# Kernel tuning notes

Hardware: AMD Instinct MI355X
Metric: run time of the kernel (lower is better)

The kernel has to match this reference:

```python
import jax, jax.numpy as jnp
import numpy as np

B, N, D = 8, 4096, 256
H = W = 64          # grid_size = img_size // patch_size = 256 // 4
WS = 8              # swin window size
NH = 8              # swin heads
M = 16              # fno modes
E = 4               # num experts
TD = 768            # text dim
HID = 1024          # mlp hidden = 4 * D
TK = 2              # top_k


def gelu(x):
    return jax.nn.gelu(x, approximate=False)


def layernorm(x, g, b, eps=1e-5):
    mu = x.mean(-1, keepdims=True)
    var = ((x - mu) ** 2).mean(-1, keepdims=True)
    return (x - mu) * jax.lax.rsqrt(var + eps) * g + b


def fno_expert(x, w1r, w1i, w2r, w2i, conv_w, conv_b):
    # x: [B, N, D] -> grid [B, D, H, W]
    xg = x.transpose(0, 2, 1).reshape(B, D, H, W)
    xft = jnp.fft.rfft2(xg)                      # [B, D, H, W//2+1] complex64
    w1 = w1r + 1j * w1i
    w2 = w2r + 1j * w2i
    top = jnp.einsum('bixy,ioxy->boxy', xft[:, :, :M, :M], w1)
    bot = jnp.einsum('bixy,ioxy->boxy', xft[:, :, -M:, :M], w2)
    out_ft = jnp.zeros((B, D, H, W // 2 + 1), dtype=xft.dtype)
    out_ft = out_ft.at[:, :, :M, :M].set(top).at[:, :, -M:, :M].set(bot)
    x1 = jnp.fft.irfft2(out_ft, s=(H, W))        # [B, D, H, W]
    x2 = jnp.einsum('bdhw,do->bohw', xg, conv_w) + conv_b[None, :, None, None]
    out = gelu(x1 + x2)
    return out.reshape(B, D, N).transpose(0, 2, 1) + x


def mlp_expert(x, w1, b1, w2, b2):
    return gelu(x @ w1 + b1) @ w2 + b2 + x


def window_attn_expert(x, ln1_g, ln1_b, qkv_w, qkv_b, out_w, out_b,
                       ln2_g, ln2_b, mw1, mb1, mw2, mb2):
    shortcut = x
    h = layernorm(x, ln1_g, ln1_b)
    # window partition: [B,H,W,C] -> [B*nW, WS*WS, C]
    h = h.reshape(B, H // WS, WS, W // WS, WS, D)
    h = h.transpose(0, 1, 3, 2, 4, 5).reshape(-1, WS * WS, D)
    # multi-head self attention (torch nn.MultiheadAttention semantics)
    qkv = h @ qkv_w + qkv_b                      # [Bw, L, 3D]
    q, k, v = jnp.split(qkv, 3, axis=-1)
    dh = D // NH
    def heads(t):
        return t.reshape(-1, WS * WS, NH, dh).transpose(0, 2, 1, 3)
    q, k, v = heads(q), heads(k), heads(v)
    scores = jnp.einsum('whld,whmd->whlm', q, k) / jnp.sqrt(jnp.float32(dh))
    attn = jax.nn.softmax(scores, axis=-1)
    o = jnp.einsum('whlm,whmd->whld', attn, v)
    o = o.transpose(0, 2, 1, 3).reshape(-1, WS * WS, D)
    o = o @ out_w + out_b
    # window reverse
    o = o.reshape(B, H // WS, W // WS, WS, WS, D)
    o = o.transpose(0, 1, 3, 2, 4, 5).reshape(B, N, D)
    x = o + shortcut
    h2 = layernorm(x, ln2_g, ln2_b)
    return x + (gelu(h2 @ mw1 + mb1) @ mw2 + mb2)


def setup_inputs() -> dict:
    key = jax.random.key(0)
    ks = jax.random.split(key, 24)
    rn = lambda k, s: jax.random.normal(k, s, jnp.float32) * 0.02
    fscale = 1.0 / (D * D)
    ru = lambda k: jax.random.uniform(k, (D, D, M, M), jnp.float32) * fscale
    return {
        'x': jax.random.normal(ks[0], (B, N, D), jnp.float32),
        'text_embedding': jax.random.normal(ks[1], (B, TD), jnp.float32),
        'gate_w1': rn(ks[2], (D + TD, D)), 'gate_b1': jnp.zeros((D,), jnp.float32),
        'gate_w2': rn(ks[3], (D, E)), 'gate_b2': jnp.zeros((E,), jnp.float32),
        'fno_w1r': ru(ks[4]), 'fno_w1i': ru(ks[5]),
        'fno_w2r': ru(ks[6]), 'fno_w2i': ru(ks[7]),
        'fno_conv_w': rn(ks[8], (D, D)), 'fno_conv_b': jnp.zeros((D,), jnp.float32),
        'mlp1_w1': rn(ks[9], (D, HID)), 'mlp1_b1': jnp.zeros((HID,), jnp.float32),
        'mlp1_w2': rn(ks[10], (HID, D)), 'mlp1_b2': jnp.zeros((D,), jnp.float32),
        'mlp2_w1': rn(ks[11], (D, HID)), 'mlp2_b1': jnp.zeros((HID,), jnp.float32),
        'mlp2_w2': rn(ks[12], (HID, D)), 'mlp2_b2': jnp.zeros((D,), jnp.float32),
        'wa_ln1_g': jnp.ones((D,), jnp.float32), 'wa_ln1_b': jnp.zeros((D,), jnp.float32),
        'wa_qkv_w': rn(ks[13], (D, 3 * D)), 'wa_qkv_b': jnp.zeros((3 * D,), jnp.float32),
        'wa_out_w': rn(ks[14], (D, D)), 'wa_out_b': jnp.zeros((D,), jnp.float32),
        'wa_ln2_g': jnp.ones((D,), jnp.float32), 'wa_ln2_b': jnp.zeros((D,), jnp.float32),
        'wa_mlp_w1': rn(ks[15], (D, HID)), 'wa_mlp_b1': jnp.zeros((HID,), jnp.float32),
        'wa_mlp_w2': rn(ks[16], (HID, D)), 'wa_mlp_b2': jnp.zeros((D,), jnp.float32),
    }


def reference(x, text_embedding, gate_w1, gate_b1, gate_w2, gate_b2,
              fno_w1r, fno_w1i, fno_w2r, fno_w2i, fno_conv_w, fno_conv_b,
              mlp1_w1, mlp1_b1, mlp1_w2, mlp1_b2,
              mlp2_w1, mlp2_b1, mlp2_w2, mlp2_b2,
              wa_ln1_g, wa_ln1_b, wa_qkv_w, wa_qkv_b, wa_out_w, wa_out_b,
              wa_ln2_g, wa_ln2_b, wa_mlp_w1, wa_mlp_b1, wa_mlp_w2, wa_mlp_b2):
    # --- gating ---
    feat = jnp.concatenate([x.mean(axis=1), text_embedding], axis=1)  # [B, D+TD]
    logits = jax.nn.relu(feat @ gate_w1 + gate_b1) @ gate_w2 + gate_b2  # [B, E]
    top_v, top_i = jax.lax.top_k(logits, TK)
    weights = jax.nn.softmax(top_v, axis=-1)                           # [B, TK]
    # per-expert combined weight: cw[b,e] = sum_k w[b,k] * (idx[b,k]==e)
    cw = (jax.nn.one_hot(top_i, E, dtype=x.dtype) * weights[..., None]).sum(axis=1)  # [B, E]
    # --- experts (FNO, MLP, WindowAttn, MLP) ---
    e0 = fno_expert(x, fno_w1r, fno_w1i, fno_w2r, fno_w2i, fno_conv_w, fno_conv_b)
    e1 = mlp_expert(x, mlp1_w1, mlp1_b1, mlp1_w2, mlp1_b2)
    e2 = window_attn_expert(x, wa_ln1_g, wa_ln1_b, wa_qkv_w, wa_qkv_b,
                            wa_out_w, wa_out_b, wa_ln2_g, wa_ln2_b,
                            wa_mlp_w1, wa_mlp_b1, wa_mlp_w2, wa_mlp_b2)
    e3 = mlp_expert(x, mlp2_w1, mlp2_b1, mlp2_w2, mlp2_b2)
    outs = jnp.stack([e0, e1, e2, e3])                                 # [E, B, N, D]
    final = jnp.einsum('be,ebnd->bnd', cw, outs)
    return final, weights
```

## Files before the change

### kernel.cpp

```cpp
#include <hip/hip_runtime.h>
#include <math.h>


#define NB 8
#define NN 4096
#define DD 256

typedef __attribute__((ext_vector_type(8))) short bf16x8;
typedef __attribute__((ext_vector_type(4))) float f32x4;

__device__ __forceinline__ float gelu_f(float v) {
    return 0.5f * v * (1.0f + erff(v * 0.7071067811865475f));
}
__device__ __forceinline__ ushort f2bf(float f) {
    uint32_t u = __float_as_uint(f);
    uint32_t r = (u + 0x7fffu + ((u >> 16) & 1u)) >> 16;
    return (ushort)r;
}
__device__ __forceinline__ float b2f(ushort h) {
    return __uint_as_float(((uint32_t)h) << 16);
}

__global__ void k_gate_mean1(const float* __restrict__ x, float* __restrict__ partial) {
    int c = blockIdx.x, b = blockIdx.y;
    int t = threadIdx.x;
    const float* xb = x + ((size_t)b * NN + c * 128) * DD;
    float s = 0.f;
    for (int n = 0; n < 128; ++n) s += xb[(size_t)n * DD + t];
    partial[((size_t)b * 32 + c) * 256 + t] = s;
}
__global__ void k_gate_mean2(const float* __restrict__ partial, const float* __restrict__ text,
                             float* __restrict__ feat) {
    int b = blockIdx.x, t = threadIdx.x;
    float s = 0.f;
    for (int c = 0; c < 32; ++c) s += partial[((size_t)b * 32 + c) * 256 + t];
    feat[b * 1024 + t] = s * (1.0f / NN);
    for (int j = t; j < 768; j += 256) feat[b * 1024 + 256 + j] = text[b * 768 + j];
}

__global__ void k_gate_mlp1(const float* __restrict__ feat, const float* __restrict__ w1,
                            const float* __restrict__ b1, float* __restrict__ h1) {
    int b = blockIdx.x, j = threadIdx.x;
    float acc = b1[j];
    const float* f = feat + b * 1024;
    for (int k = 0; k < 1024; ++k) acc += f[k] * w1[k * 256 + j];
    h1[b * 256 + j] = fmaxf(acc, 0.f);
}

__global__ void k_gate_top(const float* __restrict__ h1, const float* __restrict__ w2,
                           const float* __restrict__ b2, float* __restrict__ cw,
                           float* __restrict__ wout) {
    __shared__ float lg[8][4];
    int t = threadIdx.x;
    if (t < 32) {
        int b = t >> 2, e = t & 3;
        float acc = b2[e];
        const float* h = h1 + b * 256;
        for (int k = 0; k < 256; ++k) acc += h[k] * w2[k * 4 + e];
        lg[b][e] = acc;
    }
    __syncthreads();
    if (t < 8) {
        int b = t;
        float v[4];
        #pragma unroll
        for (int e = 0; e < 4; ++e) v[e] = lg[b][e];
        int i0 = 0;
        #pragma unroll
        for (int e = 1; e < 4; ++e) if (v[e] > v[i0]) i0 = e;
        int i1 = -1;
        #pragma unroll
        for (int e = 0; e < 4; ++e) {
            if (e == i0) continue;
            if (i1 < 0 || v[e] > v[i1]) i1 = e;
        }
        float v0 = v[i0], v1 = v[i1];
        float e1v = expf(v1 - v0);
        float inv = 1.0f / (1.0f + e1v);
        float w0 = inv, w1v = e1v * inv;
        wout[b * 2 + 0] = w0;
        wout[b * 2 + 1] = w1v;
        float c[4] = {0.f, 0.f, 0.f, 0.f};
        c[i0] += w0; c[i1] += w1v;
        #pragma unroll
        for (int e = 0; e < 4; ++e) cw[b * 4 + e] = c[e];
    }
}

__global__ void k_cvtbf(const float* __restrict__ src, ushort* __restrict__ dst) {
    int i = blockIdx.x * 256 + threadIdx.x;
    float4 v = ((const float4*)src)[i];
    ushort4 o;
    o.x = f2bf(v.x); o.y = f2bf(v.y); o.z = f2bf(v.z); o.w = f2bf(v.w);
    ((ushort4*)dst)[i] = o;
}

__global__ void k_wt(const float* __restrict__ src, ushort* __restrict__ dst, int K, int N) {
    __shared__ float tile[32][33];
    int n0 = blockIdx.x * 32, k0 = blockIdx.y * 32;
    int tx = threadIdx.x, ty = threadIdx.y;
    #pragma unroll
    for (int i = 0; i < 4; ++i)
        tile[ty + i * 8][tx] = src[(size_t)(k0 + ty + i * 8) * N + n0 + tx];
    __syncthreads();
    #pragma unroll
    for (int i = 0; i < 4; ++i)
        dst[(size_t)(n0 + ty + i * 8) * K + k0 + tx] = f2bf(tile[tx][ty + i * 8]);
}

template<int MODE>
__global__ void __launch_bounds__(256) k_gemm(const ushort* __restrict__ A,
        const ushort* __restrict__ Bt, const float* __restrict__ bias,
        const float* __restrict__ res, float* __restrict__ outf,
        ushort* __restrict__ outb, const float* __restrict__ cw, int eidx,
        int K, int Ncols, size_t bsA, size_t bsB, size_t bsC) {
    __shared__ alignas(16) char smem[32768];
    ushort* sA = (ushort*)smem;
    ushort* sB = (ushort*)(smem + 16384);
    int z = blockIdx.z;
    A += z * bsA; Bt += z * bsB;
    if (outf) outf += z * bsC;
    if (outb) outb += z * bsC;
    int m0 = blockIdx.x * 128;
    int n0 = blockIdx.y * 128;
    int t = threadIdx.x;
    int lane = t & 63, wid = t >> 6;
    int wr = wid >> 1, wc = wid & 1;
    int rlo = lane & 15, khi = (lane >> 4) * 8;

    auto stage = [&](int buf, int k0) {
        const ushort* Ab = A + (size_t)m0 * K + k0;
        const ushort* Bb = Bt + (size_t)n0 * K + k0;
        #pragma unroll
        for (int h = 0; h < 2; ++h) {
            int s = t + h * 256;
            int row = s >> 2, kc = (s & 3) * 8;
            __builtin_amdgcn_global_load_lds(
                (const __attribute__((address_space(1))) void*)(Ab + (size_t)row * K + kc),
                (__attribute__((address_space(3))) void*)(sA + buf * 4096 + s * 8),
                16, 0, 0);
            __builtin_amdgcn_global_load_lds(
                (const __attribute__((address_space(1))) void*)(Bb + (size_t)row * K + kc),
                (__attribute__((address_space(3))) void*)(sB + buf * 4096 + s * 8),
                16, 0, 0);
        }
    };

    f32x4 acc[4][4];
    #pragma unroll
    for (int i = 0; i < 4; ++i)
        #pragma unroll
        for (int j = 0; j < 4; ++j) acc[i][j] = (f32x4){0.f, 0.f, 0.f, 0.f};

    int KT = K >> 5;
    stage(0, 0);
    int cur = 0;
    for (int kt = 0; kt < KT; ++kt) {
        __syncthreads();
        if (kt + 1 < KT) stage(cur ^ 1, (kt + 1) << 5);
        const ushort* Ap = sA + cur * 4096;
        const ushort* Bp = sB + cur * 4096;
        bf16x8 af[4], bfr[4];
        #pragma unroll
        for (int i = 0; i < 4; ++i) {
            af[i]  = *(const bf16x8*)(Ap + (wr * 64 + i * 16 + rlo) * 32 + khi);
            bfr[i] = *(const bf16x8*)(Bp + (wc * 64 + i * 16 + rlo) * 32 + khi);
        }
        #pragma unroll
        for (int i = 0; i < 4; ++i)
            #pragma unroll
            for (int j = 0; j < 4; ++j)
                acc[i][j] = __builtin_amdgcn_mfma_f32_16x16x32_bf16(af[i], bfr[j], acc[i][j], 0, 0, 0);
        cur ^= 1;
    }

    float bj4[4];
    if constexpr (MODE != 4 && MODE != 5) {
        #pragma unroll
        for (int nt = 0; nt < 4; ++nt) bj4[nt] = bias[n0 + wc * 64 + nt * 16 + rlo];
    }

    if constexpr (MODE == 0 || MODE == 1 || MODE == 5) {
        ushort* eb = (ushort*)smem;
        #pragma unroll
        for (int mt = 0; mt < 4; ++mt) {
            __syncthreads();
            #pragma unroll
            for (int nt = 0; nt < 4; ++nt) {
                int col = wc * 64 + nt * 16 + rlo;
                #pragma unroll
                for (int j = 0; j < 4; ++j) {
                    float v = acc[mt][nt][j];
                    if constexpr (MODE == 5)
                        v += bias[m0 + wr * 64 + mt * 16 + (lane >> 4) * 4 + j];
                    else
                        v += bj4[nt];
                    if (MODE == 0) v = gelu_f(v);
                    eb[(wr * 16 + (lane >> 4) * 4 + j) * 136 + col] = f2bf(v);
                }
            }
            __syncthreads();
            #pragma unroll
            for (int h = 0; h < 2; ++h) {
                int s = t + h * 256;
                int r = s >> 4, c = (s & 15) * 8;
                int grow = m0 + (r >> 4) * 64 + mt * 16 + (r & 15);
                *(uint4*)(outb + (size_t)grow * Ncols + n0 + c) = *(uint4*)&eb[r * 136 + c];
            }
        }
    } else {
        float* ep = (float*)smem;
        #pragma unroll
        for (int mt = 0; mt < 4; ++mt) {
            __syncthreads();
            #pragma unroll
            for (int nt = 0; nt < 4; ++nt) {
                int col = wc * 64 + nt * 16 + rlo;
                #pragma unroll
                for (int j = 0; j < 4; ++j) {
                    float v = acc[mt][nt][j];
                    if constexpr (MODE == 4)
                        v += bias[m0 + wr * 64 + mt * 16 + (lane >> 4) * 4 + j];
                    else
                        v += bj4[nt];
                    ep[(wr * 16 + (lane >> 4) * 4 + j) * 132 + col] = v;
                }
            }
            __syncthreads();
            #pragma unroll
            for (int h = 0; h < 4; ++h) {
                int s = t + h * 256;
                int r = s >> 5, c4 = (s & 31) * 4;
                int grow = m0 + (r >> 4) * 64 + mt * 16 + (r & 15);
                size_t g = (size_t)grow * Ncols + n0 + c4;
                float4 v = *(float4*)&ep[r * 132 + c4];
                if constexpr (MODE == 2) {
                    if (res) {
                        float4 rv = *(const float4*)&res[g];
                        v.x += rv.x; v.y += rv.y; v.z += rv.z; v.w += rv.w;
                    }
                    *(float4*)&outf[g] = v;
                } else if constexpr (MODE == 4) {
                    *(float4*)&outf[g] = v;
                } else {
                    float cwv = cw[(grow >> 12) * 4 + eidx];
                    float4 rv = *(const float4*)&res[g];
                    float4 ov = *(float4*)&outf[g];
                    ov.x += cwv * (v.x + rv.x);
                    ov.y += cwv * (v.y + rv.y);
                    ov.z += cwv * (v.z + rv.z);
                    ov.w += cwv * (v.w + rv.w);
                    *(float4*)&outf[g] = ov;
                }
            }
        }
    }
}

__global__ void k_transpose(const float* __restrict__ x, float* __restrict__ xg) {
    __shared__ float tile[32][33];
    int b = blockIdx.z;
    int nt = blockIdx.x, dt = blockIdx.y;
    int tx = threadIdx.x, ty = threadIdx.y;
    const float* xb = x + (size_t)b * NN * DD;
    float* xgb = xg + (size_t)b * DD * NN;
    #pragma unroll
    for (int i = 0; i < 4; ++i) {
        int n = nt * 32 + ty + i * 8;
        tile[ty + i * 8][tx] = xb[(size_t)n * DD + dt * 32 + tx];
    }
    __syncthreads();
    #pragma unroll
    for (int i = 0; i < 4; ++i) {
        int d = dt * 32 + ty + i * 8;
        xgb[(size_t)d * NN + nt * 32 + tx] = tile[tx][ty + i * 8];
    }
}

__global__ void __launch_bounds__(64) k_rfft2(const float* __restrict__ xg, float* __restrict__ xft) {
    __shared__ float plane[64][65];
    __shared__ float s1[64][16][2];
    __shared__ float twc[64], tws[64];
    int p = blockIdx.x;
    int t = threadIdx.x;
    const float* src = xg + (size_t)p * 4096;
    for (int i = 0; i < 64; ++i) plane[i][t] = src[i * 64 + t];
    twc[t] = cosf((float)t * (6.283185307179586f / 64.0f));
    tws[t] = sinf((float)t * (6.283185307179586f / 64.0f));
    __syncthreads();
    int r = t;
    for (int kw = 0; kw < 16; ++kw) {
        float re = 0.f, im = 0.f;
        for (int w = 0; w < 64; ++w) {
            int j = (w * kw) & 63;
            float xv = plane[r][w];
            re += xv * twc[j];
            im -= xv * tws[j];
        }
        s1[r][kw][0] = re; s1[r][kw][1] = im;
    }
    __syncthreads();
    float2* dst = (float2*)xft + (size_t)p * 512;
    #pragma unroll
    for (int q = 0; q < 8; ++q) {
        int oi = t + q * 64;
        int krow = oi >> 4, kw = oi & 15;
        int kh = krow < 16 ? krow : krow + 32;
        float re = 0.f, im = 0.f;
        for (int h = 0; h < 64; ++h) {
            int j = (h * kh) & 63;
            float c = twc[j], s = tws[j];
            float ar = s1[h][kw][0], ai = s1[h][kw][1];
            re += ar * c + ai * s;
            im += ai * c - ar * s;
        }
        dst[oi] = make_float2(re, im);
    }
}

__global__ void __launch_bounds__(512) k_spectral(const float* __restrict__ xft,
        const float* __restrict__ w1r, const float* __restrict__ w1i,
        const float* __restrict__ w2r, const float* __restrict__ w2i,
        float* __restrict__ part) {
    __shared__ alignas(16) ushort Wl[32 * 648];
    __shared__ alignas(16) ushort Xl[16 * 648];
    int z = blockIdx.z;
    int region = z >> 1, is = z & 1;
    const float* wrp = region ? w2r : w1r;
    const float* wip = region ? w2i : w1i;
    int xm = blockIdx.y;
    int krow = region * 16 + xm;
    int o0 = blockIdx.x * 16;
    int t = threadIdx.x;
    int wv = t >> 6, lane = t & 63;
    int rlo = lane & 15, khi = lane >> 4;
    int ibase = is * 128;

    f32x4 acc[2][2];
    #pragma unroll
    for (int a = 0; a < 2; ++a)
        #pragma unroll
        for (int b = 0; b < 2; ++b) acc[a][b] = (f32x4){0.f, 0.f, 0.f, 0.f};

    for (int ch = 0; ch < 4; ++ch) {
        int i0 = ibase + ch * 32;
        __syncthreads();
        #pragma unroll
        for (int s = 0; s < 2; ++s) {
            int m = t + s * 512;
            int y4 = m & 3, ol = (m >> 2) & 15, i8 = (m >> 6) & 7, arr = m >> 9;
            const float* wsrc = arr ? wip : wrp;
            int ig = i0 + i8 * 4;
            float4 f[4];
            #pragma unroll
            for (int u = 0; u < 4; ++u)
                f[u] = *(const float4*)&wsrc[((size_t)(ig + u) * 256 + o0 + ol) * 256 + xm * 16 + y4 * 4];
            #pragma unroll
            for (int yy2 = 0; yy2 < 4; ++yy2) {
                int y = y4 * 4 + yy2;
                ushort4 pk;
                pk.x = f2bf(((const float*)&f[0])[yy2]);
                pk.y = f2bf(((const float*)&f[1])[yy2]);
                pk.z = f2bf(((const float*)&f[2])[yy2]);
                pk.w = f2bf(((const float*)&f[3])[yy2]);
                *(ushort4*)&Wl[(y * 2 + arr) * 648 + ol * 40 + i8 * 4] = pk;
            }
        }
        #pragma unroll
        for (int s = 0; s < 2; ++s) {
            int m = t + s * 512;
            int y = m & 15, i4 = (m >> 4) & 7, b = (m >> 7) & 7;
            int ig = i0 + i4 * 4;
            float2 g[4];
            #pragma unroll
            for (int u = 0; u < 4; ++u)
                g[u] = *(const float2*)&xft[(((size_t)(b * 256 + ig + u)) * 32 + krow) * 32 + y * 2];
            ushort4 re, im;
            re.x = f2bf(g[0].x); re.y = f2bf(g[1].x); re.z = f2bf(g[2].x); re.w = f2bf(g[3].x);
            im.x = f2bf(g[0].y); im.y = f2bf(g[1].y); im.z = f2bf(g[2].y); im.w = f2bf(g[3].y);
            *(ushort4*)&Xl[b * 648 + y * 40 + i4 * 4] = re;
            *(ushort4*)&Xl[(b + 8) * 648 + y * 40 + i4 * 4] = im;
        }
        __syncthreads();
        #pragma unroll
        for (int yy = 0; yy < 2; ++yy) {
            int y = wv * 2 + yy;
            bf16x8 Bf = *(const bf16x8*)&Xl[rlo * 648 + y * 40 + khi * 8];
            #pragma unroll
            for (int arr = 0; arr < 2; ++arr) {
                bf16x8 Af = *(const bf16x8*)&Wl[(y * 2 + arr) * 648 + rlo * 40 + khi * 8];
                acc[yy][arr] = __builtin_amdgcn_mfma_f32_16x16x32_bf16(Af, Bf, acc[yy][arr], 0, 0, 0);
            }
        }
    }

    float* dp = part + (size_t)is * 4194304;
    int c = rlo;
    int b = c & 7, hi = c >> 3;
    #pragma unroll
    for (int yy = 0; yy < 2; ++yy) {
        int y = wv * 2 + yy;
        #pragma unroll
        for (int j = 0; j < 4; ++j) {
            float C1 = acc[yy][0][j];
            float c2x = __shfl_xor(acc[yy][1][j], 8);
            float val = hi ? (c2x + C1) : (C1 - c2x);
            int o = o0 + khi * 4 + j;
            dp[(((size_t)(b * 256 + o) * 32 + krow) * 16 + y) * 2 + hi] = val;
        }
    }
}

__global__ void __launch_bounds__(64) k_irfft_fuse(const float* __restrict__ part,
        const ushort* __restrict__ x2t, ushort* __restrict__ tmp) {
    __shared__ float F[32][16][2];
    __shared__ float tarr[64][16][2];
    __shared__ float twc[64], tws[64];
    int p = blockIdx.x;
    int t = threadIdx.x;
    const float2* s0 = (const float2*)part + (size_t)p * 512;
    #pragma unroll
    for (int l = 0; l < 8; ++l) {
        int idx = t + l * 64;
        float2 a = s0[idx];
        float2 b2 = s0[idx + 2097152];
        ((float2*)F)[idx] = make_float2(a.x + b2.x, a.y + b2.y);
    }
    twc[t] = cosf((float)t * (6.283185307179586f / 64.0f));
    tws[t] = sinf((float)t * (6.283185307179586f / 64.0f));
    __syncthreads();
    int h = t;
    for (int kw = 0; kw < 16; ++kw) {
        float re = 0.f, im = 0.f;
        #pragma unroll
        for (int krow = 0; krow < 32; ++krow) {
            int kh = krow < 16 ? krow : krow + 32;
            int j = (h * kh) & 63;
            float c = twc[j], s = tws[j];
            float fr = F[krow][kw][0], fi = F[krow][kw][1];
            re += fr * c - fi * s;
            im += fr * s + fi * c;
        }
        tarr[h][kw][0] = re * (1.f / 64.f);
        tarr[h][kw][1] = im * (1.f / 64.f);
    }
    __syncthreads();
    const ushort* x2p = x2t + (size_t)p * 4096;
    ushort* tp = tmp + (size_t)p * 4096;
    for (int q = 0; q < 64; ++q) {
        int w = t;
        float acc = tarr[q][0][0];
        #pragma unroll
        for (int kw = 1; kw < 16; ++kw) {
            int j = (w * kw) & 63;
            acc += 2.f * (tarr[q][kw][0] * twc[j] - tarr[q][kw][1] * tws[j]);
        }
        float x1 = acc * (1.f / 64.f);
        int idx = q * 64 + w;
        tp[idx] = f2bf(gelu_f(x1 + b2f(x2p[idx])));
    }
}

__global__ void k_fno_final(const ushort* __restrict__ tmp, const float* __restrict__ x,
        const float* __restrict__ cw, float* __restrict__ out) {
    __shared__ float tile[32][33];
    int b = blockIdx.z;
    int n0 = blockIdx.x * 32, d0 = blockIdx.y * 32;
    int tx = threadIdx.x, ty = threadIdx.y;
    const ushort* tb = tmp + (size_t)b * DD * NN;
    #pragma unroll
    for (int i = 0; i < 4; ++i)
        tile[ty + i * 8][tx] = b2f(tb[(size_t)(d0 + ty + i * 8) * NN + n0 + tx]);
    __syncthreads();
    float cw0 = cw[b * 4];
    #pragma unroll
    for (int i = 0; i < 4; ++i) {
        int n = n0 + ty + i * 8, d = d0 + tx;
        size_t g = ((size_t)b * NN + n) * DD + d;
        out[g] = cw0 * (tile[tx][ty + i * 8] + x[g]);
    }
}

__global__ void __launch_bounds__(256) k_ln(const float* __restrict__ in, const float* __restrict__ g,
        const float* __restrict__ be, ushort* __restrict__ outb) {
    int row = blockIdx.x * 4 + (threadIdx.x >> 6);
    int lane = threadIdx.x & 63;
    const float4* rp = (const float4*)(in + (size_t)row * 256);
    float4 v = rp[lane];
    float s = v.x + v.y + v.z + v.w;
    float s2 = v.x * v.x + v.y * v.y + v.z * v.z + v.w * v.w;
    #pragma unroll
    for (int off = 32; off > 0; off >>= 1) {
        s += __shfl_down(s, off);
        s2 += __shfl_down(s2, off);
    }
    s = __shfl(s, 0); s2 = __shfl(s2, 0);
    float mu = s * (1.f / 256.f);
    float var = s2 * (1.f / 256.f) - mu * mu;
    float rstd = rsqrtf(var + 1e-5f);
    float4 gv = ((const float4*)g)[lane];
    float4 bv = ((const float4*)be)[lane];
    ushort4 ov;
    ov.x = f2bf((v.x - mu) * rstd * gv.x + bv.x);
    ov.y = f2bf((v.y - mu) * rstd * gv.y + bv.y);
    ov.z = f2bf((v.z - mu) * rstd * gv.z + bv.z);
    ov.w = f2bf((v.w - mu) * rstd * gv.w + bv.w);
    ((ushort4*)(outb + (size_t)row * 256))[lane] = ov;
}

__global__ void __launch_bounds__(256) k_window_attn(const ushort* __restrict__ qkvb,
        ushort* __restrict__ aob) {
    __shared__ ushort lds[4 * 7424];
    int t = threadIdx.x;
    int w = t >> 6, lane = t & 63;
    int wi = blockIdx.x, hh = blockIdx.y;
    int hd = hh * 4 + w;
    int b = wi >> 6, hb = (wi >> 3) & 7, wb = wi & 7;
    ushort* A = lds + w * 7424;
    ushort* Kl = A + 2560;
    ushort* Vt = A + 5120;
    int rlo = lane & 15, kq = lane >> 4;

    int tok = lane;
    int n = hb * 512 + wb * 8 + ((tok >> 3) << 6) + (tok & 7);
    const ushort* gq = qkvb + ((size_t)b * 4096 + n) * 768 + hd * 32;
    const uint4* qp = (const uint4*)gq;
    const uint4* kp = (const uint4*)(gq + 256);
    const uint4* vp = (const uint4*)(gq + 512);
    uint4 q0 = qp[0], q1 = qp[1], q2 = qp[2], q3 = qp[3];
    uint4 k0 = kp[0], k1 = kp[1], k2 = kp[2], k3 = kp[3];
    uint4 v0 = vp[0], v1 = vp[1], v2 = vp[2], v3 = vp[3];
    uint4* qr = (uint4*)(A + tok * 40);
    qr[0] = q0; qr[1] = q1; qr[2] = q2; qr[3] = q3;
    uint4* kr = (uint4*)(Kl + tok * 40);
    kr[0] = k0; kr[1] = k1; kr[2] = k2; kr[3] = k3;
    ushort vbuf[32];
    *(uint4*)&vbuf[0] = v0; *(uint4*)&vbuf[8] = v1;
    *(uint4*)&vbuf[16] = v2; *(uint4*)&vbuf[24] = v3;
    #pragma unroll
    for (int d = 0; d < 32; ++d) Vt[d * 72 + tok] = vbuf[d];
    __syncthreads();

    bf16x8 Qf[4], Kf[4];
    #pragma unroll
    for (int lt = 0; lt < 4; ++lt)
        Qf[lt] = *(const bf16x8*)(A + (lt * 16 + rlo) * 40 + kq * 8);
    #pragma unroll
    for (int mt = 0; mt < 4; ++mt)
        Kf[mt] = *(const bf16x8*)(Kl + (mt * 16 + rlo) * 40 + kq * 8);

    f32x4 S[4][4];
    #pragma unroll
    for (int lt = 0; lt < 4; ++lt)
        #pragma unroll
        for (int mt = 0; mt < 4; ++mt)
            S[lt][mt] = __builtin_amdgcn_mfma_f32_16x16x32_bf16(Qf[lt], Kf[mt],
                        (f32x4){0.f, 0.f, 0.f, 0.f}, 0, 0, 0);
    __syncthreads();

    const float scale = 0.17677669529663687f;
    float inv_[4][4];
    #pragma unroll
    for (int lt = 0; lt < 4; ++lt) {
        float m4[4], s4[4];
        #pragma unroll
        for (int j = 0; j < 4; ++j) {
            m4[j] = fmaxf(fmaxf(S[lt][0][j], S[lt][1][j]), fmaxf(S[lt][2][j], S[lt][3][j]));
        }
        #pragma unroll
        for (int off = 1; off < 16; off <<= 1)
            #pragma unroll
            for (int j = 0; j < 4; ++j) m4[j] = fmaxf(m4[j], __shfl_xor(m4[j], off));
        #pragma unroll
        for (int j = 0; j < 4; ++j) s4[j] = 0.f;
        #pragma unroll
        for (int mt = 0; mt < 4; ++mt)
            #pragma unroll
            for (int j = 0; j < 4; ++j) {
                float p = expf((S[lt][mt][j] - m4[j]) * scale);
                s4[j] += p;
                A[(lt * 16 + kq * 4 + j) * 72 + mt * 16 + rlo] = f2bf(p);
            }
        #pragma unroll
        for (int off = 1; off < 16; off <<= 1)
            #pragma unroll
            for (int j = 0; j < 4; ++j) s4[j] += __shfl_xor(s4[j], off);
        #pragma unroll
        for (int j = 0; j < 4; ++j) inv_[lt][j] = 1.0f / s4[j];
    }
    __syncthreads();

    f32x4 O[4][2];
    #pragma unroll
    for (int lt = 0; lt < 4; ++lt)
        #pragma unroll
        for (int dt = 0; dt < 2; ++dt) {
            f32x4 o = (f32x4){0.f, 0.f, 0.f, 0.f};
            #pragma unroll
            for (int mc = 0; mc < 2; ++mc) {
                bf16x8 pa = *(const bf16x8*)(A + (lt * 16 + rlo) * 72 + mc * 32 + kq * 8);
                bf16x8 vb = *(const bf16x8*)(Vt + (dt * 16 + rlo) * 72 + mc * 32 + kq * 8);
                o = __builtin_amdgcn_mfma_f32_16x16x32_bf16(pa, vb, o, 0, 0, 0);
            }
            O[lt][dt] = o;
        }
    __syncthreads();

    #pragma unroll
    for (int lt = 0; lt < 4; ++lt)
        #pragma unroll
        for (int dt = 0; dt < 2; ++dt)
            #pragma unroll
            for (int j = 0; j < 4; ++j)
                A[(lt * 16 + kq * 4 + j) * 40 + dt * 16 + rlo] = f2bf(O[lt][dt][j] * inv_[lt][j]);
    __syncthreads();
    const uint4* orow = (const uint4*)(A + lane * 40);
    uint4 o0 = orow[0], o1 = orow[1], o2 = orow[2], o3 = orow[3];
    uint4* gout = (uint4*)(aob + ((size_t)b * 4096 + n) * 256 + hd * 32);
    gout[0] = o0; gout[1] = o1; gout[2] = o2; gout[3] = o3;
}

extern "C" void kernel_launch(void* const* d_in, const int* in_sizes, int n_in,
                              void* d_out, int out_size, void* d_ws, size_t ws_size,
                              hipStream_t stream) {
    (void)in_sizes; (void)n_in; (void)out_size; (void)ws_size;
    const float* x        = (const float*)d_in[0];
    const float* text     = (const float*)d_in[1];
    const float* gate_w1  = (const float*)d_in[2];
    const float* gate_b1  = (const float*)d_in[3];
    const float* gate_w2  = (const float*)d_in[4];
    const float* gate_b2  = (const float*)d_in[5];
    const float* fno_w1r  = (const float*)d_in[6];
    const float* fno_w1i  = (const float*)d_in[7];
    const float* fno_w2r  = (const float*)d_in[8];
    const float* fno_w2i  = (const float*)d_in[9];
    const float* fno_cw   = (const float*)d_in[10];
    const float* fno_cb   = (const float*)d_in[11];
    const float* mlp1_w1  = (const float*)d_in[12];
    const float* mlp1_b1  = (const float*)d_in[13];
    const float* mlp1_w2  = (const float*)d_in[14];
    const float* mlp1_b2  = (const float*)d_in[15];
    const float* mlp2_w1  = (const float*)d_in[16];
    const float* mlp2_b1  = (const float*)d_in[17];
    const float* mlp2_w2  = (const float*)d_in[18];
    const float* mlp2_b2  = (const float*)d_in[19];
    const float* ln1_g    = (const float*)d_in[20];
    const float* ln1_b    = (const float*)d_in[21];
    const float* qkv_w    = (const float*)d_in[22];
    const float* qkv_b    = (const float*)d_in[23];
    const float* out_w    = (const float*)d_in[24];
    const float* out_b    = (const float*)d_in[25];
    const float* ln2_g    = (const float*)d_in[26];
    const float* ln2_b    = (const float*)d_in[27];
    const float* wa_w1    = (const float*)d_in[28];
    const float* wa_b1    = (const float*)d_in[29];
    const float* wa_w2    = (const float*)d_in[30];
    const float* wa_b2    = (const float*)d_in[31];

    float* ws   = (float*)d_ws;
    float* feat = ws;
    float* h1   = ws + 8192;
    float* cwp  = ws + 10240;
    ushort* wbf = (ushort*)(ws + 16384);
    ushort* w1aT = wbf;
    ushort* w2aT = w1aT + 262144;
    ushort* w1bT = w2aT + 262144;
    ushort* w2bT = w1bT + 262144;
    ushort* w1cT = w2bT + 262144;
    ushort* w2cT = w1cT + 262144;
    ushort* qkvT = w2cT + 262144;
    ushort* outwT = qkvT + 196608;
    ushort* convT = outwT + 65536;
    ushort* Xbf  = (ushort*)(ws + 16384 + 1048576);
    float* slotA = ws + 16384 + 1048576 + 4194304;
    ushort* abf  = (ushort*)slotA;
    float* xft   = slotA + 8388608;
    float* oft   = xft + 2097152;
    float* regD  = oft + 2097152;
    ushort* bigb = (ushort*)(regD + 8388608);
    float* gpart = oft;

    float* outp = (float*)d_out;
    float* wout = outp + (size_t)NB * NN * DD;

    k_gate_mean1<<<dim3(32, 8), 256, 0, stream>>>(x, gpart);
    k_gate_mean2<<<8, 256, 0, stream>>>(gpart, text, feat);
    k_gate_mlp1<<<8, 256, 0, stream>>>(feat, gate_w1, gate_b1, h1);
    k_gate_top<<<1, 64, 0, stream>>>(h1, gate_w2, gate_b2, cwp, wout);

    k_cvtbf<<<8192, 256, 0, stream>>>(x, Xbf);
    dim3 wtb(32, 8);
    k_wt<<<dim3(32, 8), wtb, 0, stream>>>(mlp1_w1, w1aT, 256, 1024);
    k_wt<<<dim3(8, 32), wtb, 0, stream>>>(mlp1_w2, w2aT, 1024, 256);
    k_wt<<<dim3(32, 8), wtb, 0, stream>>>(mlp2_w1, w1bT, 256, 1024);
    k_wt<<<dim3(8, 32), wtb, 0, stream>>>(mlp2_w2, w2bT, 1024, 256);
    k_wt<<<dim3(32, 8), wtb, 0, stream>>>(wa_w1, w1cT, 256, 1024);
    k_wt<<<dim3(8, 32), wtb, 0, stream>>>(wa_w2, w2cT, 1024, 256);
    k_wt<<<dim3(24, 8), wtb, 0, stream>>>(qkv_w, qkvT, 256, 768);
    k_wt<<<dim3(8, 8), wtb, 0, stream>>>(out_w, outwT, 256, 256);
    k_wt<<<dim3(8, 8), wtb, 0, stream>>>(fno_cw, convT, 256, 256);

    k_transpose<<<dim3(128, 8, 8), dim3(32, 8), 0, stream>>>(x, slotA);
    k_rfft2<<<2048, 64, 0, stream>>>(slotA, xft);
    k_gemm<5><<<dim3(2, 32, 8), 256, 0, stream>>>(convT, Xbf, fno_cb, nullptr, nullptr,
        (ushort*)regD, nullptr, 0, 256, 4096, 0, (size_t)NN * DD, (size_t)DD * NN);
    k_spectral<<<dim3(16, 16, 4), 512, 0, stream>>>(xft, fno_w1r, fno_w1i, fno_w2r, fno_w2i, slotA);
    k_irfft_fuse<<<2048, 64, 0, stream>>>(slotA, (const ushort*)regD, bigb);
    k_fno_final<<<dim3(128, 8, 8), dim3(32, 8), 0, stream>>>(bigb, x, cwp, outp);

    k_gemm<0><<<dim3(256, 8), 256, 0, stream>>>(Xbf, w1aT, mlp1_b1, nullptr, nullptr, bigb, nullptr, 0, 256, 1024, 0, 0, 0);
    k_gemm<3><<<dim3(256, 2), 256, 0, stream>>>(bigb, w2aT, mlp1_b2, x, outp, nullptr, cwp, 1, 1024, 256, 0, 0, 0);

    k_ln<<<8192, 256, 0, stream>>>(x, ln1_g, ln1_b, abf);
    k_gemm<1><<<dim3(256, 6), 256, 0, stream>>>(abf, qkvT, qkv_b, nullptr, nullptr, bigb, nullptr, 0, 256, 768, 0, 0, 0);
    k_window_attn<<<dim3(512, 2), 256, 0, stream>>>(bigb, abf);
    k_gemm<2><<<dim3(256, 2), 256, 0, stream>>>(abf, outwT, out_b, x, regD, nullptr, nullptr, 0, 256, 256, 0, 0, 0);
    k_ln<<<8192, 256, 0, stream>>>(regD, ln2_g, ln2_b, abf);
    k_gemm<0><<<dim3(256, 8), 256, 0, stream>>>(abf, w1cT, wa_b1, nullptr, nullptr, bigb, nullptr, 0, 256, 1024, 0, 0, 0);
    k_gemm<3><<<dim3(256, 2), 256, 0, stream>>>(bigb, w2cT, wa_b2, regD, outp, nullptr, cwp, 2, 1024, 256, 0, 0, 0);

    k_gemm<0><<<dim3(256, 8), 256, 0, stream>>>(Xbf, w1bT, mlp2_b1, nullptr, nullptr, bigb, nullptr, 0, 256, 1024, 0, 0, 0);
    k_gemm<3><<<dim3(256, 2), 256, 0, stream>>>(bigb, w2bT, mlp2_b2, x, outp, nullptr, cwp, 3, 1024, 256, 0, 0, 0);
}
```

Baseline: 694.9 us.

## Fuse gate mean into bf16 convert, bf16 FNO transpose, widen FFT blocks

The separate gate-mean pass is folded into the fp32-to-bf16 conversion kernel, which now also writes per-block partial sums. The FNO path transposes bf16 data instead of fp32, and the residual in the final FNO step is read from bf16. The rfft2 and irfft kernels move from 64 to 256 threads per block, with shared arrays laid out as split re/im planes. This cuts global traffic and raises occupancy, at the cost of bf16 rounding on the FNO input and residual, and a larger final reduction over 1024 partials per batch.

```diff
diff --git a/kernel.cpp b/kernel.cpp
--- a/kernel.cpp
+++ b/kernel.cpp
@@ -21,20 +21,41 @@
     return __uint_as_float(((uint32_t)h) << 16);
 }
 
-__global__ void k_gate_mean1(const float* __restrict__ x, float* __restrict__ partial) {
-    int c = blockIdx.x, b = blockIdx.y;
+__global__ void k_cvt_gate(const float* __restrict__ src, ushort* __restrict__ dst,
+                           float* __restrict__ gp) {
+    __shared__ float4 st[4][64];
+    int blk = blockIdx.x;
     int t = threadIdx.x;
-    const float* xb = x + ((size_t)b * NN + c * 128) * DD;
-    float s = 0.f;
-    for (int n = 0; n < 128; ++n) s += xb[(size_t)n * DD + t];
-    partial[((size_t)b * 32 + c) * 256 + t] = s;
-}
-__global__ void k_gate_mean2(const float* __restrict__ partial, const float* __restrict__ text,
+    int i = blk * 256 + t;
+    float4 v = ((const float4*)src)[i];
+    ushort4 o;
+    o.x = f2bf(v.x); o.y = f2bf(v.y); o.z = f2bf(v.z); o.w = f2bf(v.w);
+    ((ushort4*)dst)[i] = o;
+    st[t >> 6][t & 63] = v;
+    __syncthreads();
+    if (t < 64) {
+        float4 a = st[0][t], b = st[1][t], c = st[2][t], d = st[3][t];
+        float4 s;
+        s.x = a.x + b.x + c.x + d.x;
+        s.y = a.y + b.y + c.y + d.y;
+        s.z = a.z + b.z + c.z + d.z;
+        s.w = a.w + b.w + c.w + d.w;
+        ((float4*)(gp + (size_t)blk * 256))[t] = s;
+    }
+}
+
+__global__ void k_gate_mean2(const float* __restrict__ gp, const float* __restrict__ text,
                              float* __restrict__ feat) {
     int b = blockIdx.x, t = threadIdx.x;
-    float s = 0.f;
-    for (int c = 0; c < 32; ++c) s += partial[((size_t)b * 32 + c) * 256 + t];
-    feat[b * 1024 + t] = s * (1.0f / NN);
+    const float* base = gp + (size_t)b * 1024 * 256;
+    float s0 = 0.f, s1 = 0.f, s2 = 0.f, s3 = 0.f;
+    for (int j = 0; j < 1024; j += 4) {
+        s0 += base[(j + 0) * 256 + t];
+        s1 += base[(j + 1) * 256 + t];
+        s2 += base[(j + 2) * 256 + t];
+        s3 += base[(j + 3) * 256 + t];
+    }
+    feat[b * 1024 + t] = (s0 + s1 + s2 + s3) * (1.0f / NN);
     for (int j = t; j < 768; j += 256) feat[b * 1024 + 256 + j] = text[b * 768 + j];
 }
 
@@ -85,14 +106,6 @@
         #pragma unroll
         for (int e = 0; e < 4; ++e) cw[b * 4 + e] = c[e];
     }
-}
-
-__global__ void k_cvtbf(const float* __restrict__ src, ushort* __restrict__ dst) {
-    int i = blockIdx.x * 256 + threadIdx.x;
-    float4 v = ((const float4*)src)[i];
-    ushort4 o;
-    o.x = f2bf(v.x); o.y = f2bf(v.y); o.z = f2bf(v.z); o.w = f2bf(v.w);
-    ((ushort4*)dst)[i] = o;
 }
 
 __global__ void k_wt(const float* __restrict__ src, ushort* __restrict__ dst, int K, int N) {
@@ -257,13 +270,13 @@
     }
 }
 
-__global__ void k_transpose(const float* __restrict__ x, float* __restrict__ xg) {
-    __shared__ float tile[32][33];
+__global__ void k_transpose(const ushort* __restrict__ x, ushort* __restrict__ xg) {
+    __shared__ ushort tile[32][34];
     int b = blockIdx.z;
     int nt = blockIdx.x, dt = blockIdx.y;
     int tx = threadIdx.x, ty = threadIdx.y;
-    const float* xb = x + (size_t)b * NN * DD;
-    float* xgb = xg + (size_t)b * DD * NN;
+    const ushort* xb = x + (size_t)b * NN * DD;
+    ushort* xgb = xg + (size_t)b * DD * NN;
     #pragma unroll
     for (int i = 0; i < 4; ++i) {
         int n = nt * 32 + ty + i * 8;
@@ -277,19 +290,28 @@
     }
 }
 
-__global__ void __launch_bounds__(64) k_rfft2(const float* __restrict__ xg, float* __restrict__ xft) {
+__global__ void __launch_bounds__(256) k_rfft2(const ushort* __restrict__ xg, float* __restrict__ xft) {
     __shared__ float plane[64][65];
-    __shared__ float s1[64][16][2];
+    __shared__ float s1re[16][66], s1im[16][66];
     __shared__ float twc[64], tws[64];
     int p = blockIdx.x;
     int t = threadIdx.x;
-    const float* src = xg + (size_t)p * 4096;
-    for (int i = 0; i < 64; ++i) plane[i][t] = src[i * 64 + t];
-    twc[t] = cosf((float)t * (6.283185307179586f / 64.0f));
-    tws[t] = sinf((float)t * (6.283185307179586f / 64.0f));
-    __syncthreads();
-    int r = t;
-    for (int kw = 0; kw < 16; ++kw) {
+    int tx = t & 63, grp = t >> 6;
+    const ushort* src = xg + (size_t)p * 4096;
+    #pragma unroll
+    for (int i = 0; i < 16; ++i) {
+        int row = grp * 16 + i;
+        plane[row][tx] = b2f(src[row * 64 + tx]);
+    }
+    if (t < 64) {
+        twc[t] = cosf((float)t * (6.283185307179586f / 64.0f));
+        tws[t] = sinf((float)t * (6.283185307179586f / 64.0f));
+    }
+    __syncthreads();
+    int r = tx;
+    #pragma unroll
+    for (int q = 0; q < 4; ++q) {
+        int kw = grp + q * 4;
         float re = 0.f, im = 0.f;
         for (int w = 0; w < 64; ++w) {
             int j = (w * kw) & 63;
@@ -297,20 +319,21 @@
             re += xv * twc[j];
             im -= xv * tws[j];
         }
-        s1[r][kw][0] = re; s1[r][kw][1] = im;
+        s1re[kw][r] = re;
+        s1im[kw][r] = im;
     }
     __syncthreads();
     float2* dst = (float2*)xft + (size_t)p * 512;
     #pragma unroll
-    for (int q = 0; q < 8; ++q) {
-        int oi = t + q * 64;
+    for (int q = 0; q < 2; ++q) {
+        int oi = t + q * 256;
         int krow = oi >> 4, kw = oi & 15;
         int kh = krow < 16 ? krow : krow + 32;
         float re = 0.f, im = 0.f;
         for (int h = 0; h < 64; ++h) {
             int j = (h * kh) & 63;
             float c = twc[j], s = tws[j];
-            float ar = s1[h][kw][0], ai = s1[h][kw][1];
+            float ar = s1re[kw][h], ai = s1im[kw][h];
             re += ar * c + ai * s;
             im += ai * c - ar * s;
         }
@@ -395,8 +418,7 @@
     }
 
     float* dp = part + (size_t)is * 4194304;
-    int c = rlo;
-    int b = c & 7, hi = c >> 3;
+    int b = rlo & 7, hi = rlo >> 3;
     #pragma unroll
     for (int yy = 0; yy < 2; ++yy) {
         int y = wv * 2 + yy;
@@ -411,26 +433,30 @@
     }
 }
 
-__global__ void __launch_bounds__(64) k_irfft_fuse(const float* __restrict__ part,
+__global__ void __launch_bounds__(256) k_irfft_fuse(const float* __restrict__ part,
         const ushort* __restrict__ x2t, ushort* __restrict__ tmp) {
     __shared__ float F[32][16][2];
-    __shared__ float tarr[64][16][2];
+    __shared__ float tre[16][66], tim[16][66];
     __shared__ float twc[64], tws[64];
     int p = blockIdx.x;
     int t = threadIdx.x;
     const float2* s0 = (const float2*)part + (size_t)p * 512;
     #pragma unroll
-    for (int l = 0; l < 8; ++l) {
-        int idx = t + l * 64;
+    for (int l = 0; l < 2; ++l) {
+        int idx = t + l * 256;
         float2 a = s0[idx];
         float2 b2 = s0[idx + 2097152];
         ((float2*)F)[idx] = make_float2(a.x + b2.x, a.y + b2.y);
     }
-    twc[t] = cosf((float)t * (6.283185307179586f / 64.0f));
-    tws[t] = sinf((float)t * (6.283185307179586f / 64.0f));
-    __syncthreads();
-    int h = t;
-    for (int kw = 0; kw < 16; ++kw) {
+    if (t < 64) {
+        twc[t] = cosf((float)t * (6.283185307179586f / 64.0f));
+        tws[t] = sinf((float)t * (6.283185307179586f / 64.0f));
+    }
+    __syncthreads();
+    int h = t & 63;
+    #pragma unroll
+    for (int q = 0; q < 4; ++q) {
+        int kw = (t >> 6) + q * 4;
         float re = 0.f, im = 0.f;
         #pragma unroll
         for (int krow = 0; krow < 32; ++krow) {
@@ -441,27 +467,29 @@
             re += fr * c - fi * s;
             im += fr * s + fi * c;
         }
-        tarr[h][kw][0] = re * (1.f / 64.f);
-        tarr[h][kw][1] = im * (1.f / 64.f);
+        tre[kw][h] = re * (1.f / 64.f);
+        tim[kw][h] = im * (1.f / 64.f);
     }
     __syncthreads();
     const ushort* x2p = x2t + (size_t)p * 4096;
     ushort* tp = tmp + (size_t)p * 4096;
-    for (int q = 0; q < 64; ++q) {
-        int w = t;
-        float acc = tarr[q][0][0];
+    int w = t & 63;
+    #pragma unroll
+    for (int qq = 0; qq < 16; ++qq) {
+        int qrow = (t >> 6) + qq * 4;
+        float acc = tre[0][qrow];
         #pragma unroll
         for (int kw = 1; kw < 16; ++kw) {
             int j = (w * kw) & 63;
-            acc += 2.f * (tarr[q][kw][0] * twc[j] - tarr[q][kw][1] * tws[j]);
+            acc += 2.f * (tre[kw][qrow] * twc[j] - tim[kw][qrow] * tws[j]);
         }
         float x1 = acc * (1.f / 64.f);
-        int idx = q * 64 + w;
+        int idx = qrow * 64 + w;
         tp[idx] = f2bf(gelu_f(x1 + b2f(x2p[idx])));
     }
 }
 
-__global__ void k_fno_final(const ushort* __restrict__ tmp, const float* __restrict__ x,
+__global__ void k_fno_final(const ushort* __restrict__ tmp, const ushort* __restrict__ xbf,
         const float* __restrict__ cw, float* __restrict__ out) {
     __shared__ float tile[32][33];
     int b = blockIdx.z;
@@ -477,7 +505,7 @@
     for (int i = 0; i < 4; ++i) {
         int n = n0 + ty + i * 8, d = d0 + tx;
         size_t g = ((size_t)b * NN + n) * DD + d;
-        out[g] = cw0 * (tile[tx][ty + i * 8] + x[g]);
+        out[g] = cw0 * (tile[tx][ty + i * 8] + b2f(xbf[g]));
     }
 }
 
@@ -683,12 +711,11 @@
     float* outp = (float*)d_out;
     float* wout = outp + (size_t)NB * NN * DD;
 
-    k_gate_mean1<<<dim3(32, 8), 256, 0, stream>>>(x, gpart);
+    k_cvt_gate<<<8192, 256, 0, stream>>>(x, Xbf, gpart);
     k_gate_mean2<<<8, 256, 0, stream>>>(gpart, text, feat);
     k_gate_mlp1<<<8, 256, 0, stream>>>(feat, gate_w1, gate_b1, h1);
     k_gate_top<<<1, 64, 0, stream>>>(h1, gate_w2, gate_b2, cwp, wout);
 
-    k_cvtbf<<<8192, 256, 0, stream>>>(x, Xbf);
     dim3 wtb(32, 8);
     k_wt<<<dim3(32, 8), wtb, 0, stream>>>(mlp1_w1, w1aT, 256, 1024);
     k_wt<<<dim3(8, 32), wtb, 0, stream>>>(mlp1_w2, w2aT, 1024, 256);
@@ -700,13 +727,13 @@
     k_wt<<<dim3(8, 8), wtb, 0, stream>>>(out_w, outwT, 256, 256);
     k_wt<<<dim3(8, 8), wtb, 0, stream>>>(fno_cw, convT, 256, 256);
 
-    k_transpose<<<dim3(128, 8, 8), dim3(32, 8), 0, stream>>>(x, slotA);
-    k_rfft2<<<2048, 64, 0, stream>>>(slotA, xft);
+    k_transpose<<<dim3(128, 8, 8), dim3(32, 8), 0, stream>>>(Xbf, (ushort*)slotA);
+    k_rfft2<<<2048, 256, 0, stream>>>((const ushort*)slotA, xft);
     k_gemm<5><<<dim3(2, 32, 8), 256, 0, stream>>>(convT, Xbf, fno_cb, nullptr, nullptr,
         (ushort*)regD, nullptr, 0, 256, 4096, 0, (size_t)NN * DD, (size_t)DD * NN);
     k_spectral<<<dim3(16, 16, 4), 512, 0, stream>>>(xft, fno_w1r, fno_w1i, fno_w2r, fno_w2i, slotA);
-    k_irfft_fuse<<<2048, 64, 0, stream>>>(slotA, (const ushort*)regD, bigb);
-    k_fno_final<<<dim3(128, 8, 8), dim3(32, 8), 0, stream>>>(bigb, x, cwp, outp);
+    k_irfft_fuse<<<2048, 256, 0, stream>>>(slotA, (const ushort*)regD, bigb);
+    k_fno_final<<<dim3(128, 8, 8), dim3(32, 8), 0, stream>>>(bigb, Xbf, cwp, outp);
 
     k_gemm<0><<<dim3(256, 8), 256, 0, stream>>>(Xbf, w1aT, mlp1_b1, nullptr, nullptr, bigb, nullptr, 0, 256, 1024, 0, 0, 0);
     k_gemm<3><<<dim3(256, 2), 256, 0, stream>>>(bigb, w2aT, mlp1_b2, x, outp, nullptr, cwp, 1, 1024, 256, 0, 0, 0);
```

Result: no change. 700.5 us (+0.8%).
